# Performance work log

Hardware: AMD Instinct MI355X
Metric: run time of the kernel (lower is better)

## Reference

```python
import jax, jax.numpy as jnp
import numpy as np

IN_CH = 256
HID = 64
HEADS = 3 * 0 + 4  # num_heads


def setup_inputs() -> dict:
    key = jax.random.key(0)
    ks = jax.random.split(key, 5)
    B, C, H, W = 2, IN_CH, 64, 64
    x = jax.random.normal(ks[0], (B, C, H, W), dtype=jnp.float32)
    # per-head embed conv (kernel 1 -> stored as [heads, 3*HID, C]); kaiming fan_out-ish scale
    w_embed = jax.random.normal(ks[1], (HEADS, 3 * HID, C), dtype=jnp.float32) * np.float32(np.sqrt(2.0 / (3 * HID)))
    b_embed = jnp.zeros((HEADS, 3 * HID), dtype=jnp.float32)
    # output ConvTranspose2d(hidden*heads -> C, kernel 1): weight [hidden*heads, C]
    w_out = jax.random.normal(ks[2], (HEADS * HID, C), dtype=jnp.float32) * np.float32(np.sqrt(2.0 / C))
    b_out = jnp.zeros((C,), dtype=jnp.float32)
    return {"x": x, "w_embed": w_embed, "b_embed": b_embed, "w_out": w_out, "b_out": b_out}


def reference(x, w_embed, b_embed, w_out, b_out):
    B, C, H, W = x.shape
    N = H * W
    nH = w_embed.shape[0]
    D = w_embed.shape[1] // 3
    scale = D ** -0.5
    # 1x1 embed conv per head: [B, nH, 3D, N]
    xf = x.reshape(B, C, N)
    qkv = jnp.einsum('bcn,hdc->bhdn', xf, w_embed) + b_embed[None, :, :, None]
    q, k, v = jnp.split(qkv, 3, axis=2)  # each [B, nH, D, N]
    attn = jnp.einsum('bhci,bhcj->bhij', q, k) * scale  # [B, nH, N, N]
    attn = jax.nn.softmax(attn, axis=-1)
    y = jnp.einsum('bhij,bhcj->bhci', attn, v)  # [B, nH, D, N]
    y = y.reshape(B, nH * D, N)
    # output 1x1 transposed conv (kernel 1 == plain 1x1 projection)
    out = jnp.einsum('bkn,kc->bcn', y, w_out) + b_out[None, :, None]
    out = out.reshape(B, C, H, W)
    return out + x  # residual
```

## Files before the change

kernel.cpp:

```cpp
#include <hip/hip_runtime.h>
#include <hip/hip_bf16.h>

#define NH   4
#define D_   64
#define N_   4096
#define C_   256
#define ME   768
#define SPLITS 3

typedef float    f32x4  __attribute__((ext_vector_type(4)));
typedef float    f32x16 __attribute__((ext_vector_type(16)));
typedef _Float16 f16x8  __attribute__((ext_vector_type(8)));
typedef _Float16 f16x4  __attribute__((ext_vector_type(4)));
typedef _Float16 f16x2  __attribute__((ext_vector_type(2)));

__global__ __launch_bounds__(256) void xt_prep(const float* __restrict__ x,
                                               _Float16* __restrict__ xT) {
    __shared__ float T[64][68];
    const int n0 = blockIdx.x * 64, c0 = blockIdx.y * 64, b = blockIdx.z;
    const int t = threadIdx.x;
    const float* xp = x + ((size_t)b * C_ + c0) * N_ + n0;
    #pragma unroll
    for (int r = 0; r < 4; ++r) {
        int idx = r * 256 + t;
        int c = idx >> 4, ng = (idx & 15) * 4;
        *(f32x4*)&T[c][ng] = *(const f32x4*)(xp + (size_t)c * N_ + ng);
    }
    __syncthreads();
    _Float16* dp = xT + ((size_t)b * N_ + n0) * C_ + c0;
    #pragma unroll
    for (int r = 0; r < 2; ++r) {
        int idx = r * 256 + t;
        int n = idx >> 3, cg = (idx & 7) * 8;
        f16x8 v;
        #pragma unroll
        for (int j = 0; j < 8; ++j) v[j] = (_Float16)T[cg + j][n];
        *(f16x8*)(dp + (size_t)n * C_ + cg) = v;
    }
}

__global__ __launch_bounds__(256) void w_prep(const float* __restrict__ w_embed,
                                              const float* __restrict__ w_out,
                                              _Float16* __restrict__ wh,
                                              _Float16* __restrict__ w_outT) {
    __shared__ float T[64][68];
    const int t = threadIdx.x;
    if (blockIdx.x < 96) {
        int gid = blockIdx.x * 256 + t;
        const float* s = w_embed + (size_t)gid * 8;
        f32x4 a = *(const f32x4*)s, b2 = *(const f32x4*)(s + 4);
        f16x8 v = { (_Float16)a[0], (_Float16)a[1], (_Float16)a[2], (_Float16)a[3],
                    (_Float16)b2[0], (_Float16)b2[1], (_Float16)b2[2], (_Float16)b2[3] };
        *(f16x8*)(wh + (size_t)gid * 8) = v;
    } else {
        int tile = blockIdx.x - 96;
        int tc = tile & 3, tk = tile >> 2;
        #pragma unroll
        for (int r = 0; r < 4; ++r) {
            int idx = r * 256 + t;
            int kl = idx >> 4, cl = (idx & 15) * 4;
            *(f32x4*)&T[kl][cl] = *(const f32x4*)(w_out + (size_t)(tk * 64 + kl) * C_ + tc * 64 + cl);
        }
        __syncthreads();
        #pragma unroll
        for (int r = 0; r < 2; ++r) {
            int idx = r * 256 + t;
            int cl = idx >> 3, kg = (idx & 7) * 8;
            f16x8 v;
            #pragma unroll
            for (int j = 0; j < 8; ++j) v[j] = (_Float16)T[kg + j][cl];
            *(f16x8*)(w_outT + (size_t)(tc * 64 + cl) * C_ + tk * 64 + kg) = v;
        }
    }
}

__global__ __launch_bounds__(256) void qkv_gemm(const _Float16* __restrict__ xT,
                                                const _Float16* __restrict__ wh,
                                                const float* __restrict__ b_embed,
                                                _Float16* __restrict__ qT,
                                                _Float16* __restrict__ kT,
                                                _Float16* __restrict__ vB) {
    __shared__ __align__(16) union SM {
        struct { _Float16 A[64][40], X[64][40]; } s;
        float Os[64][68];
    } sm;
    const int n0 = blockIdx.x * 64, mt = blockIdx.y, b = blockIdx.z;
    const int m0 = mt * 64;
    const int t = threadIdx.x;
    const int lane = t & 63, w = t >> 6, quad = lane >> 4, l16 = lane & 15;
    const int srow = t >> 2, skoff = (t & 3) * 8;
    f32x4 acc[4] = {};
    for (int k0 = 0; k0 < C_; k0 += 32) {
        __syncthreads();
        *(f16x8*)&sm.s.A[srow][skoff] = *(const f16x8*)(wh + (size_t)(m0 + srow) * C_ + k0 + skoff);
        *(f16x8*)&sm.s.X[srow][skoff] = *(const f16x8*)(xT + ((size_t)b * N_ + n0 + srow) * C_ + k0 + skoff);
        __syncthreads();
        f16x8 af = *(const f16x8*)&sm.s.A[w * 16 + l16][quad * 8];
        #pragma unroll
        for (int nb = 0; nb < 4; ++nb) {
            f16x8 bf = *(const f16x8*)&sm.s.X[nb * 16 + l16][quad * 8];
            acc[nb] = __builtin_amdgcn_mfma_f32_16x16x32_f16(af, bf, acc[nb], 0, 0, 0);
        }
    }
    float bias[4];
    #pragma unroll
    for (int rg = 0; rg < 4; ++rg) bias[rg] = b_embed[m0 + w * 16 + quad * 4 + rg];
    __syncthreads();
    #pragma unroll
    for (int nb = 0; nb < 4; ++nb)
        #pragma unroll
        for (int rg = 0; rg < 4; ++rg)
            sm.Os[w * 16 + quad * 4 + rg][nb * 16 + l16] = acc[nb][rg] + bias[rg];
    __syncthreads();
    const int h = mt / 3, r3 = mt - h * 3;
    const int bh = b * NH + h;
    if (r3 < 2) {
        _Float16* dst = (r3 ? kT : qT) + ((size_t)bh * N_ + n0) * D_;
        #pragma unroll
        for (int r = 0; r < 2; ++r) {
            int idx = r * 256 + t;
            int n = idx >> 3, mg = (idx & 7) * 8;
            f16x8 v;
            #pragma unroll
            for (int j = 0; j < 8; ++j) v[j] = (_Float16)sm.Os[mg + j][n];
            *(f16x8*)(dst + (size_t)n * D_ + mg) = v;
        }
    } else {
        _Float16* dst = vB + (size_t)bh * D_ * N_ + n0;
        #pragma unroll
        for (int r = 0; r < 2; ++r) {
            int idx = r * 256 + t;
            int d = idx >> 3, ng = (idx & 7) * 8;
            f32x4 a = *(const f32x4*)&sm.Os[d][ng];
            f32x4 b2 = *(const f32x4*)&sm.Os[d][ng + 4];
            f16x8 v = { (_Float16)a[0], (_Float16)a[1], (_Float16)a[2], (_Float16)a[3],
                        (_Float16)b2[0], (_Float16)b2[1], (_Float16)b2[2], (_Float16)b2[3] };
            *(f16x8*)(dst + (size_t)d * N_ + ng) = v;
        }
    }
}

__global__ __launch_bounds__(256) void attn_kernel(const _Float16* __restrict__ qT,
                                                   const _Float16* __restrict__ kT,
                                                   const _Float16* __restrict__ vB,
                                                   _Float16* __restrict__ opart,
                                                   float* __restrict__ mpart,
                                                   float* __restrict__ lpart) {
    __shared__ __align__(16) union SM {
        struct { _Float16 K[64][76], V[64][76]; } s;
        _Float16 Os[128][76];
    } sm;
    const int t = threadIdx.x;
    const int qt = blockIdx.x, h = blockIdx.y;
    const int b = blockIdx.z / SPLITS, s = blockIdx.z % SPLITS;
    const int bh = b * NH + h, sbh = s * 8 + bh;
    const _Float16* kp = kT + (size_t)bh * N_ * D_;
    const _Float16* vp = vB + (size_t)bh * D_ * N_;
    const int lane = t & 63, w = t >> 6, l32 = lane & 31, hl = lane >> 5;
    const bool hl1 = (hl != 0);
    const int srow = t >> 3, scol = (t & 7) * 8;

    const _Float16* qp = qT + ((size_t)bh * N_ + qt * 128 + w * 32 + l32) * D_;
    f16x8 qf[4];
    #pragma unroll
    for (int kc = 0; kc < 4; ++kc) {
        qf[kc] = *(const f16x8*)(qp + kc * 16 + hl * 8);
        qf[kc] *= (_Float16)0.18033688f;
    }

    f32x16 oacc0 = {}, oacc1 = {};
    float m_run = -3.0e38f, l_run = 0.f;

    const int jt_lo = (s * 64) / SPLITS, jt_hi = ((s + 1) * 64) / SPLITS;
    f16x8 kpre[2], vpre[2];
    #pragma unroll
    for (int r = 0; r < 2; ++r) {
        int row = srow + r * 32;
        kpre[r] = *(const f16x8*)(kp + (size_t)(jt_lo * 64 + row) * D_ + scol);
        vpre[r] = *(const f16x8*)(vp + (size_t)row * N_ + jt_lo * 64 + scol);
    }

    for (int jt = jt_lo; jt < jt_hi; ++jt) {
        __syncthreads();
        #pragma unroll
        for (int r = 0; r < 2; ++r) {
            int row = srow + r * 32;
            *(f16x8*)&sm.s.K[row][scol] = kpre[r];
            *(f16x8*)&sm.s.V[row][scol] = vpre[r];
        }
        __syncthreads();
        if (jt + 1 < jt_hi) {
            #pragma unroll
            for (int r = 0; r < 2; ++r) {
                int row = srow + r * 32;
                kpre[r] = *(const f16x8*)(kp + (size_t)((jt + 1) * 64 + row) * D_ + scol);
                vpre[r] = *(const f16x8*)(vp + (size_t)row * N_ + (jt + 1) * 64 + scol);
            }
        }

        f32x16 sa0 = {}, sa1 = {};
        #pragma unroll
        for (int kc = 0; kc < 4; ++kc) {
            f16x8 kf0 = *(const f16x8*)&sm.s.K[l32][kc * 16 + hl * 8];
            sa0 = __builtin_amdgcn_mfma_f32_32x32x16_f16(kf0, qf[kc], sa0, 0, 0, 0);
            f16x8 kf1 = *(const f16x8*)&sm.s.K[32 + l32][kc * 16 + hl * 8];
            sa1 = __builtin_amdgcn_mfma_f32_32x32x16_f16(kf1, qf[kc], sa1, 0, 0, 0);
        }

        float mx = fmaxf(sa0[0], sa0[1]);
        #pragma unroll
        for (int r = 2; r < 16; ++r) mx = fmaxf(mx, sa0[r]);
        #pragma unroll
        for (int r = 0; r < 16; ++r) mx = fmaxf(mx, sa1[r]);
        mx = fmaxf(mx, __shfl_xor(mx, 32));
        float mnew  = fmaxf(m_run, mx);
        float alpha = exp2f(m_run - mnew);
        float rs = 0.f;
        #pragma unroll
        for (int r = 0; r < 16; ++r) { sa0[r] = exp2f(sa0[r] - mnew); rs += sa0[r]; }
        #pragma unroll
        for (int r = 0; r < 16; ++r) { sa1[r] = exp2f(sa1[r] - mnew); rs += sa1[r]; }
        rs += __shfl_xor(rs, 32);
        l_run = l_run * alpha + rs;
        m_run = mnew;
        #pragma unroll
        for (int r = 0; r < 16; ++r) { oacc0[r] *= alpha; oacc1[r] *= alpha; }

        #pragma unroll
        for (int jb = 0; jb < 2; ++jb) {
            const f32x16& sa = jb ? sa1 : sa0;
            int P[8], X[8];
            #pragma unroll
            for (int q = 0; q < 8; ++q) {
                f16x2 pk = { (_Float16)sa[2 * q], (_Float16)sa[2 * q + 1] };
                P[q] = __builtin_bit_cast(int, pk);
            }
            #pragma unroll
            for (int q = 0; q < 8; ++q) X[q] = __shfl_xor(P[q], 32);
            union FU { f16x8 v; int d[4]; } f0, f1;
            f0.d[0] = hl1 ? X[2] : P[0];
            f0.d[1] = hl1 ? X[3] : P[1];
            f0.d[2] = hl1 ? P[2] : X[0];
            f0.d[3] = hl1 ? P[3] : X[1];
            f1.d[0] = hl1 ? X[6] : P[4];
            f1.d[1] = hl1 ? X[7] : P[5];
            f1.d[2] = hl1 ? P[6] : X[4];
            f1.d[3] = hl1 ? P[7] : X[5];
            f16x8 vf = *(const f16x8*)&sm.s.V[l32][jb * 32 + hl * 8];
            oacc0 = __builtin_amdgcn_mfma_f32_32x32x16_f16(vf, f0.v, oacc0, 0, 0, 0);
            vf = *(const f16x8*)&sm.s.V[l32][jb * 32 + 16 + hl * 8];
            oacc0 = __builtin_amdgcn_mfma_f32_32x32x16_f16(vf, f1.v, oacc0, 0, 0, 0);
            vf = *(const f16x8*)&sm.s.V[32 + l32][jb * 32 + hl * 8];
            oacc1 = __builtin_amdgcn_mfma_f32_32x32x16_f16(vf, f0.v, oacc1, 0, 0, 0);
            vf = *(const f16x8*)&sm.s.V[32 + l32][jb * 32 + 16 + hl * 8];
            oacc1 = __builtin_amdgcn_mfma_f32_32x32x16_f16(vf, f1.v, oacc1, 0, 0, 0);
        }
    }

    float linv = 1.f / l_run;
    if (hl == 0) {
        mpart[(size_t)sbh * N_ + qt * 128 + w * 32 + l32] = m_run;
        lpart[(size_t)sbh * N_ + qt * 128 + w * 32 + l32] = l_run;
    }
    __syncthreads();
    #pragma unroll
    for (int db = 0; db < 2; ++db) {
        const f32x16& oc = db ? oacc1 : oacc0;
        #pragma unroll
        for (int rq = 0; rq < 4; ++rq) {
            f16x4 pv = { (_Float16)(oc[rq * 4 + 0] * linv), (_Float16)(oc[rq * 4 + 1] * linv),
                         (_Float16)(oc[rq * 4 + 2] * linv), (_Float16)(oc[rq * 4 + 3] * linv) };
            *(f16x4*)&sm.Os[w * 32 + l32][db * 32 + rq * 8 + hl * 4] = pv;
        }
    }
    __syncthreads();
    _Float16* op = opart + ((size_t)sbh * N_ + qt * 128) * D_;
    #pragma unroll
    for (int r = 0; r < 4; ++r) {
        int idx = r * 256 + t;
        int i = idx >> 3, ch = (idx & 7) * 8;
        *(f16x8*)(op + (size_t)i * D_ + ch) = *(const f16x8*)&sm.Os[i][ch];
    }
}

__global__ __launch_bounds__(256) void combine_kernel(const _Float16* __restrict__ opart,
                                                      const float* __restrict__ mpart,
                                                      const float* __restrict__ lpart,
                                                      _Float16* __restrict__ yT) {
    const int bhi = blockIdx.y;
    const int idx = blockIdx.x * 256 + threadIdx.x;
    const int n = idx >> 3, dg = (idx & 7) * 8;
    const int b = bhi >> 2, h = bhi & 3;
    float m0 = mpart[(size_t)bhi * N_ + n];
    float m1 = mpart[(size_t)(8 + bhi) * N_ + n];
    float m2 = mpart[(size_t)(16 + bhi) * N_ + n];
    float l0 = lpart[(size_t)bhi * N_ + n];
    float l1 = lpart[(size_t)(8 + bhi) * N_ + n];
    float l2 = lpart[(size_t)(16 + bhi) * N_ + n];
    float M  = fmaxf(m0, fmaxf(m1, m2));
    float w0 = exp2f(m0 - M) * l0, w1 = exp2f(m1 - M) * l1, w2 = exp2f(m2 - M) * l2;
    float inv = 1.f / (w0 + w1 + w2);
    w0 *= inv; w1 *= inv; w2 *= inv;
    f16x8 o0 = *(const f16x8*)(opart + ((size_t)bhi * N_ + n) * D_ + dg);
    f16x8 o1 = *(const f16x8*)(opart + ((size_t)(8 + bhi) * N_ + n) * D_ + dg);
    f16x8 o2 = *(const f16x8*)(opart + ((size_t)(16 + bhi) * N_ + n) * D_ + dg);
    f16x8 v;
    #pragma unroll
    for (int j = 0; j < 8; ++j)
        v[j] = (_Float16)(w0 * (float)o0[j] + w1 * (float)o1[j] + w2 * (float)o2[j]);
    *(f16x8*)(yT + ((size_t)b * N_ + n) * C_ + h * 64 + dg) = v;
}

__global__ __launch_bounds__(256) void proj_gemm(const _Float16* __restrict__ yT,
                                                 const _Float16* __restrict__ w_outT,
                                                 const float* __restrict__ b_out,
                                                 const float* __restrict__ x,
                                                 float* __restrict__ out) {
    __shared__ __align__(16) union SM {
        struct { _Float16 A[64][40], Y[64][40]; } s;
        float Os[64][68];
    } sm;
    const int n0 = blockIdx.x * 64, c0 = blockIdx.y * 64, b = blockIdx.z;
    const int t = threadIdx.x;
    const int lane = t & 63, w = t >> 6, quad = lane >> 4, l16 = lane & 15;
    const int srow = t >> 2, skoff = (t & 3) * 8;
    f32x4 acc[4] = {};
    for (int k0 = 0; k0 < C_; k0 += 32) {
        __syncthreads();
        *(f16x8*)&sm.s.A[srow][skoff] = *(const f16x8*)(w_outT + (size_t)(c0 + srow) * C_ + k0 + skoff);
        *(f16x8*)&sm.s.Y[srow][skoff] = *(const f16x8*)(yT + ((size_t)b * N_ + n0 + srow) * C_ + k0 + skoff);
        __syncthreads();
        f16x8 af = *(const f16x8*)&sm.s.A[w * 16 + l16][quad * 8];
        #pragma unroll
        for (int nb = 0; nb < 4; ++nb) {
            f16x8 bf = *(const f16x8*)&sm.s.Y[nb * 16 + l16][quad * 8];
            acc[nb] = __builtin_amdgcn_mfma_f32_16x16x32_f16(af, bf, acc[nb], 0, 0, 0);
        }
    }
    float bias[4];
    #pragma unroll
    for (int rg = 0; rg < 4; ++rg) bias[rg] = b_out[c0 + w * 16 + quad * 4 + rg];
    __syncthreads();
    #pragma unroll
    for (int nb = 0; nb < 4; ++nb)
        #pragma unroll
        for (int rg = 0; rg < 4; ++rg)
            sm.Os[w * 16 + quad * 4 + rg][nb * 16 + l16] = acc[nb][rg] + bias[rg];
    __syncthreads();
    const float* xp = x + ((size_t)b * C_ + c0) * N_ + n0;
    float* op = out + ((size_t)b * C_ + c0) * N_ + n0;
    #pragma unroll
    for (int r = 0; r < 4; ++r) {
        int idx = r * 256 + t;
        int c = idx >> 4, ng = (idx & 15) * 4;
        f32x4 v  = *(const f32x4*)&sm.Os[c][ng];
        f32x4 xv = *(const f32x4*)(xp + (size_t)c * N_ + ng);
        f32x4 o  = { v[0] + xv[0], v[1] + xv[1], v[2] + xv[2], v[3] + xv[3] };
        *(f32x4*)(op + (size_t)c * N_ + ng) = o;
    }
}

extern "C" void kernel_launch(void* const* d_in, const int* in_sizes, int n_in,
                              void* d_out, int out_size, void* d_ws, size_t ws_size,
                              hipStream_t stream) {
    const float* x       = (const float*)d_in[0];
    const float* w_embed = (const float*)d_in[1];
    const float* b_embed = (const float*)d_in[2];
    const float* w_out   = (const float*)d_in[3];
    const float* b_out   = (const float*)d_in[4];
    float* out = (float*)d_out;

    _Float16* base   = (_Float16*)d_ws;
    _Float16* xT     = base;
    _Float16* wh     = base + 2097152;
    _Float16* w_outT = base + 2293760;
    _Float16* qT     = base + 2359296;
    _Float16* kT     = base + 4456448;
    _Float16* vB     = base + 6553600;
    _Float16* yT     = base + 8650752;
    _Float16* opart  = base + 10747904;
    float*    mpart  = (float*)(base + 17039360);
    float*    lpart  = mpart + 98304;

    xt_prep       <<<dim3(64, 4, 2),  256, 0, stream>>>(x, xT);
    w_prep        <<<dim3(112, 1, 1), 256, 0, stream>>>(w_embed, w_out, wh, w_outT);
    qkv_gemm      <<<dim3(64, 12, 2), 256, 0, stream>>>(xT, wh, b_embed, qT, kT, vB);
    attn_kernel   <<<dim3(32, 4, 6),  256, 0, stream>>>(qT, kT, vB, opart, mpart, lpart);
    combine_kernel<<<dim3(128, 8, 1), 256, 0, stream>>>(opart, mpart, lpart, yT);
    proj_gemm     <<<dim3(64, 4, 2),  256, 0, stream>>>(yT, w_outT, b_out, x, out);
}
```

Baseline: 169.1 us.

## Fuse prep kernels, fold combine into projection, double-buffer attention K/V, split-4

```diff
diff --git a/kernel.cpp b/kernel.cpp
--- a/kernel.cpp
+++ b/kernel.cpp
@@ -6,54 +6,51 @@
 #define N_   4096
 #define C_   256
 #define ME   768
-#define SPLITS 3
+#define SPLITS 4
+#define QSCALE 0.18033688f
 
 typedef float    f32x4  __attribute__((ext_vector_type(4)));
 typedef float    f32x16 __attribute__((ext_vector_type(16)));
 typedef _Float16 f16x8  __attribute__((ext_vector_type(8)));
 typedef _Float16 f16x4  __attribute__((ext_vector_type(4)));
-typedef _Float16 f16x2  __attribute__((ext_vector_type(2)));
-
-__global__ __launch_bounds__(256) void xt_prep(const float* __restrict__ x,
-                                               _Float16* __restrict__ xT) {
+
+__global__ __launch_bounds__(256) void prep_kernel(const float* __restrict__ x,
+                                                   const float* __restrict__ w_embed,
+                                                   const float* __restrict__ w_out,
+                                                   _Float16* __restrict__ xT,
+                                                   _Float16* __restrict__ wh,
+                                                   _Float16* __restrict__ w_outT) {
     __shared__ float T[64][68];
-    const int n0 = blockIdx.x * 64, c0 = blockIdx.y * 64, b = blockIdx.z;
-    const int t = threadIdx.x;
-    const float* xp = x + ((size_t)b * C_ + c0) * N_ + n0;
-    #pragma unroll
-    for (int r = 0; r < 4; ++r) {
-        int idx = r * 256 + t;
-        int c = idx >> 4, ng = (idx & 15) * 4;
-        *(f32x4*)&T[c][ng] = *(const f32x4*)(xp + (size_t)c * N_ + ng);
-    }
-    __syncthreads();
-    _Float16* dp = xT + ((size_t)b * N_ + n0) * C_ + c0;
-    #pragma unroll
-    for (int r = 0; r < 2; ++r) {
-        int idx = r * 256 + t;
-        int n = idx >> 3, cg = (idx & 7) * 8;
-        f16x8 v;
-        #pragma unroll
-        for (int j = 0; j < 8; ++j) v[j] = (_Float16)T[cg + j][n];
-        *(f16x8*)(dp + (size_t)n * C_ + cg) = v;
-    }
-}
-
-__global__ __launch_bounds__(256) void w_prep(const float* __restrict__ w_embed,
-                                              const float* __restrict__ w_out,
-                                              _Float16* __restrict__ wh,
-                                              _Float16* __restrict__ w_outT) {
-    __shared__ float T[64][68];
-    const int t = threadIdx.x;
-    if (blockIdx.x < 96) {
-        int gid = blockIdx.x * 256 + t;
+    const int t = threadIdx.x, bx = blockIdx.x;
+    if (bx < 512) {
+        const int n0 = (bx & 63) * 64, c0 = ((bx >> 6) & 3) * 64, b = bx >> 8;
+        const float* xp = x + ((size_t)b * C_ + c0) * N_ + n0;
+        #pragma unroll
+        for (int r = 0; r < 4; ++r) {
+            int idx = r * 256 + t;
+            int c = idx >> 4, ng = (idx & 15) * 4;
+            *(f32x4*)&T[c][ng] = *(const f32x4*)(xp + (size_t)c * N_ + ng);
+        }
+        __syncthreads();
+        _Float16* dp = xT + ((size_t)b * N_ + n0) * C_ + c0;
+        #pragma unroll
+        for (int r = 0; r < 2; ++r) {
+            int idx = r * 256 + t;
+            int n = idx >> 3, cg = (idx & 7) * 8;
+            f16x8 v;
+            #pragma unroll
+            for (int j = 0; j < 8; ++j) v[j] = (_Float16)T[cg + j][n];
+            *(f16x8*)(dp + (size_t)n * C_ + cg) = v;
+        }
+    } else if (bx < 608) {
+        int gid = (bx - 512) * 256 + t;
         const float* s = w_embed + (size_t)gid * 8;
         f32x4 a = *(const f32x4*)s, b2 = *(const f32x4*)(s + 4);
         f16x8 v = { (_Float16)a[0], (_Float16)a[1], (_Float16)a[2], (_Float16)a[3],
                     (_Float16)b2[0], (_Float16)b2[1], (_Float16)b2[2], (_Float16)b2[3] };
         *(f16x8*)(wh + (size_t)gid * 8) = v;
     } else {
-        int tile = blockIdx.x - 96;
+        int tile = bx - 608;
         int tc = tile & 3, tk = tile >> 2;
         #pragma unroll
         for (int r = 0; r < 4; ++r) {
@@ -89,6 +86,8 @@
     const int t = threadIdx.x;
     const int lane = t & 63, w = t >> 6, quad = lane >> 4, l16 = lane & 15;
     const int srow = t >> 2, skoff = (t & 3) * 8;
+    const int h = mt / 3, r3 = mt - h * 3;
+    const float oscale = (r3 == 0) ? QSCALE : 1.0f;
     f32x4 acc[4] = {};
     for (int k0 = 0; k0 < C_; k0 += 32) {
         __syncthreads();
@@ -110,9 +109,8 @@
     for (int nb = 0; nb < 4; ++nb)
         #pragma unroll
         for (int rg = 0; rg < 4; ++rg)
-            sm.Os[w * 16 + quad * 4 + rg][nb * 16 + l16] = acc[nb][rg] + bias[rg];
-    __syncthreads();
-    const int h = mt / 3, r3 = mt - h * 3;
+            sm.Os[w * 16 + quad * 4 + rg][nb * 16 + l16] = (acc[nb][rg] + bias[rg]) * oscale;
+    __syncthreads();
     const int bh = b * NH + h;
     if (r3 < 2) {
         _Float16* dst = (r3 ? kT : qT) + ((size_t)bh * N_ + n0) * D_;
@@ -140,19 +138,19 @@
     }
 }
 
-__global__ __launch_bounds__(256) void attn_kernel(const _Float16* __restrict__ qT,
-                                                   const _Float16* __restrict__ kT,
-                                                   const _Float16* __restrict__ vB,
-                                                   _Float16* __restrict__ opart,
-                                                   float* __restrict__ mpart,
-                                                   float* __restrict__ lpart) {
+__global__ __launch_bounds__(256, 4) void attn_kernel(const _Float16* __restrict__ qT,
+                                                      const _Float16* __restrict__ kT,
+                                                      const _Float16* __restrict__ vB,
+                                                      _Float16* __restrict__ opart,
+                                                      float* __restrict__ mpart,
+                                                      float* __restrict__ lpart) {
     __shared__ __align__(16) union SM {
-        struct { _Float16 K[64][76], V[64][76]; } s;
+        struct { _Float16 K[2][64][76], V[2][64][76]; } s;
         _Float16 Os[128][76];
     } sm;
     const int t = threadIdx.x;
     const int qt = blockIdx.x, h = blockIdx.y;
-    const int b = blockIdx.z / SPLITS, s = blockIdx.z % SPLITS;
+    const int b = blockIdx.z >> 2, s = blockIdx.z & 3;
     const int bh = b * NH + h, sbh = s * 8 + bh;
     const _Float16* kp = kT + (size_t)bh * N_ * D_;
     const _Float16* vp = vB + (size_t)bh * D_ * N_;
@@ -163,15 +161,12 @@
     const _Float16* qp = qT + ((size_t)bh * N_ + qt * 128 + w * 32 + l32) * D_;
     f16x8 qf[4];
     #pragma unroll
-    for (int kc = 0; kc < 4; ++kc) {
-        qf[kc] = *(const f16x8*)(qp + kc * 16 + hl * 8);
-        qf[kc] *= (_Float16)0.18033688f;
-    }
+    for (int kc = 0; kc < 4; ++kc) qf[kc] = *(const f16x8*)(qp + kc * 16 + hl * 8);
 
     f32x16 oacc0 = {}, oacc1 = {};
     float m_run = -3.0e38f, l_run = 0.f;
 
-    const int jt_lo = (s * 64) / SPLITS, jt_hi = ((s + 1) * 64) / SPLITS;
+    const int jt_lo = s * 16, jt_hi = jt_lo + 16;
     f16x8 kpre[2], vpre[2];
     #pragma unroll
     for (int r = 0; r < 2; ++r) {
@@ -179,17 +174,18 @@
         kpre[r] = *(const f16x8*)(kp + (size_t)(jt_lo * 64 + row) * D_ + scol);
         vpre[r] = *(const f16x8*)(vp + (size_t)row * N_ + jt_lo * 64 + scol);
     }
-
+    #pragma unroll
+    for (int r = 0; r < 2; ++r) {
+        int row = srow + r * 32;
+        *(f16x8*)&sm.s.K[0][row][scol] = kpre[r];
+        *(f16x8*)&sm.s.V[0][row][scol] = vpre[r];
+    }
+
+    int buf = 0;
     for (int jt = jt_lo; jt < jt_hi; ++jt) {
         __syncthreads();
-        #pragma unroll
-        for (int r = 0; r < 2; ++r) {
-            int row = srow + r * 32;
-            *(f16x8*)&sm.s.K[row][scol] = kpre[r];
-            *(f16x8*)&sm.s.V[row][scol] = vpre[r];
-        }
-        __syncthreads();
-        if (jt + 1 < jt_hi) {
+        const bool more = (jt + 1 < jt_hi);
+        if (more) {
             #pragma unroll
             for (int r = 0; r < 2; ++r) {
                 int row = srow + r * 32;
@@ -201,40 +197,45 @@
         f32x16 sa0 = {}, sa1 = {};
         #pragma unroll
         for (int kc = 0; kc < 4; ++kc) {
-            f16x8 kf0 = *(const f16x8*)&sm.s.K[l32][kc * 16 + hl * 8];
+            f16x8 kf0 = *(const f16x8*)&sm.s.K[buf][l32][kc * 16 + hl * 8];
             sa0 = __builtin_amdgcn_mfma_f32_32x32x16_f16(kf0, qf[kc], sa0, 0, 0, 0);
-            f16x8 kf1 = *(const f16x8*)&sm.s.K[32 + l32][kc * 16 + hl * 8];
+            f16x8 kf1 = *(const f16x8*)&sm.s.K[buf][32 + l32][kc * 16 + hl * 8];
             sa1 = __builtin_amdgcn_mfma_f32_32x32x16_f16(kf1, qf[kc], sa1, 0, 0, 0);
         }
 
-        float mx = fmaxf(sa0[0], sa0[1]);
-        #pragma unroll
-        for (int r = 2; r < 16; ++r) mx = fmaxf(mx, sa0[r]);
-        #pragma unroll
-        for (int r = 0; r < 16; ++r) mx = fmaxf(mx, sa1[r]);
+        f32x16 mm;
+        #pragma unroll
+        for (int r = 0; r < 16; ++r) mm[r] = fmaxf(sa0[r], sa1[r]);
+        f32x4 m4;
+        #pragma unroll
+        for (int r = 0; r < 4; ++r)
+            m4[r] = fmaxf(fmaxf(mm[r], mm[r + 4]), fmaxf(mm[r + 8], mm[r + 12]));
+        float mx = fmaxf(fmaxf(m4[0], m4[1]), fmaxf(m4[2], m4[3]));
         mx = fmaxf(mx, __shfl_xor(mx, 32));
         float mnew  = fmaxf(m_run, mx);
         float alpha = exp2f(m_run - mnew);
-        float rs = 0.f;
-        #pragma unroll
-        for (int r = 0; r < 16; ++r) { sa0[r] = exp2f(sa0[r] - mnew); rs += sa0[r]; }
-        #pragma unroll
-        for (int r = 0; r < 16; ++r) { sa1[r] = exp2f(sa1[r] - mnew); rs += sa1[r]; }
+        #pragma unroll
+        for (int r = 0; r < 16; ++r) sa0[r] = exp2f(sa0[r] - mnew);
+        #pragma unroll
+        for (int r = 0; r < 16; ++r) sa1[r] = exp2f(sa1[r] - mnew);
+        f32x16 sv = sa0 + sa1;
+        f32x4 s4;
+        #pragma unroll
+        for (int r = 0; r < 4; ++r) s4[r] = (sv[r] + sv[r + 4]) + (sv[r + 8] + sv[r + 12]);
+        float rs = (s4[0] + s4[1]) + (s4[2] + s4[3]);
         rs += __shfl_xor(rs, 32);
         l_run = l_run * alpha + rs;
         m_run = mnew;
-        #pragma unroll
-        for (int r = 0; r < 16; ++r) { oacc0[r] *= alpha; oacc1[r] *= alpha; }
+        oacc0 *= alpha;
+        oacc1 *= alpha;
 
         #pragma unroll
         for (int jb = 0; jb < 2; ++jb) {
             const f32x16& sa = jb ? sa1 : sa0;
             int P[8], X[8];
             #pragma unroll
-            for (int q = 0; q < 8; ++q) {
-                f16x2 pk = { (_Float16)sa[2 * q], (_Float16)sa[2 * q + 1] };
-                P[q] = __builtin_bit_cast(int, pk);
-            }
+            for (int q = 0; q < 8; ++q)
+                P[q] = __builtin_bit_cast(int, __builtin_amdgcn_cvt_pkrtz(sa[2 * q], sa[2 * q + 1]));
             #pragma unroll
             for (int q = 0; q < 8; ++q) X[q] = __shfl_xor(P[q], 32);
             union FU { f16x8 v; int d[4]; } f0, f1;
@@ -246,15 +247,25 @@
             f1.d[1] = hl1 ? X[7] : P[5];
             f1.d[2] = hl1 ? P[6] : X[4];
             f1.d[3] = hl1 ? P[7] : X[5];
-            f16x8 vf = *(const f16x8*)&sm.s.V[l32][jb * 32 + hl * 8];
+            f16x8 vf = *(const f16x8*)&sm.s.V[buf][l32][jb * 32 + hl * 8];
             oacc0 = __builtin_amdgcn_mfma_f32_32x32x16_f16(vf, f0.v, oacc0, 0, 0, 0);
-            vf = *(const f16x8*)&sm.s.V[l32][jb * 32 + 16 + hl * 8];
+            vf = *(const f16x8*)&sm.s.V[buf][l32][jb * 32 + 16 + hl * 8];
             oacc0 = __builtin_amdgcn_mfma_f32_32x32x16_f16(vf, f1.v, oacc0, 0, 0, 0);
-            vf = *(const f16x8*)&sm.s.V[32 + l32][jb * 32 + hl * 8];
+            vf = *(const f16x8*)&sm.s.V[buf][32 + l32][jb * 32 + hl * 8];
             oacc1 = __builtin_amdgcn_mfma_f32_32x32x16_f16(vf, f0.v, oacc1, 0, 0, 0);
-            vf = *(const f16x8*)&sm.s.V[32 + l32][jb * 32 + 16 + hl * 8];
+            vf = *(const f16x8*)&sm.s.V[buf][32 + l32][jb * 32 + 16 + hl * 8];
             oacc1 = __builtin_amdgcn_mfma_f32_32x32x16_f16(vf, f1.v, oacc1, 0, 0, 0);
         }
+
+        if (more) {
+            #pragma unroll
+            for (int r = 0; r < 2; ++r) {
+                int row = srow + r * 32;
+                *(f16x8*)&sm.s.K[buf ^ 1][row][scol] = kpre[r];
+                *(f16x8*)&sm.s.V[buf ^ 1][row][scol] = vpre[r];
+            }
+        }
+        buf ^= 1;
     }
 
     float linv = 1.f / l_run;
@@ -283,52 +294,62 @@
     }
 }
 
-__global__ __launch_bounds__(256) void combine_kernel(const _Float16* __restrict__ opart,
-                                                      const float* __restrict__ mpart,
-                                                      const float* __restrict__ lpart,
-                                                      _Float16* __restrict__ yT) {
-    const int bhi = blockIdx.y;
-    const int idx = blockIdx.x * 256 + threadIdx.x;
-    const int n = idx >> 3, dg = (idx & 7) * 8;
-    const int b = bhi >> 2, h = bhi & 3;
-    float m0 = mpart[(size_t)bhi * N_ + n];
-    float m1 = mpart[(size_t)(8 + bhi) * N_ + n];
-    float m2 = mpart[(size_t)(16 + bhi) * N_ + n];
-    float l0 = lpart[(size_t)bhi * N_ + n];
-    float l1 = lpart[(size_t)(8 + bhi) * N_ + n];
-    float l2 = lpart[(size_t)(16 + bhi) * N_ + n];
-    float M  = fmaxf(m0, fmaxf(m1, m2));
-    float w0 = exp2f(m0 - M) * l0, w1 = exp2f(m1 - M) * l1, w2 = exp2f(m2 - M) * l2;
-    float inv = 1.f / (w0 + w1 + w2);
-    w0 *= inv; w1 *= inv; w2 *= inv;
-    f16x8 o0 = *(const f16x8*)(opart + ((size_t)bhi * N_ + n) * D_ + dg);
-    f16x8 o1 = *(const f16x8*)(opart + ((size_t)(8 + bhi) * N_ + n) * D_ + dg);
-    f16x8 o2 = *(const f16x8*)(opart + ((size_t)(16 + bhi) * N_ + n) * D_ + dg);
-    f16x8 v;
-    #pragma unroll
-    for (int j = 0; j < 8; ++j)
-        v[j] = (_Float16)(w0 * (float)o0[j] + w1 * (float)o1[j] + w2 * (float)o2[j]);
-    *(f16x8*)(yT + ((size_t)b * N_ + n) * C_ + h * 64 + dg) = v;
-}
-
-__global__ __launch_bounds__(256) void proj_gemm(const _Float16* __restrict__ yT,
+__global__ __launch_bounds__(256) void proj_gemm(const _Float16* __restrict__ opart,
+                                                 const float* __restrict__ mpart,
+                                                 const float* __restrict__ lpart,
                                                  const _Float16* __restrict__ w_outT,
                                                  const float* __restrict__ b_out,
                                                  const float* __restrict__ x,
                                                  float* __restrict__ out) {
     __shared__ __align__(16) union SM {
-        struct { _Float16 A[64][40], Y[64][40]; } s;
+        struct { _Float16 A[64][40], Y[64][40]; float W[4][64][4]; } s;
         float Os[64][68];
     } sm;
     const int n0 = blockIdx.x * 64, c0 = blockIdx.y * 64, b = blockIdx.z;
     const int t = threadIdx.x;
     const int lane = t & 63, w = t >> 6, quad = lane >> 4, l16 = lane & 15;
     const int srow = t >> 2, skoff = (t & 3) * 8;
+
+    {
+        const int nl = t & 63, hh = t >> 6;
+        const int bh = b * NH + hh;
+        float mv[4], lv[4];
+        #pragma unroll
+        for (int sI = 0; sI < 4; ++sI) {
+            mv[sI] = mpart[(size_t)(sI * 8 + bh) * N_ + n0 + nl];
+            lv[sI] = lpart[(size_t)(sI * 8 + bh) * N_ + n0 + nl];
+        }
+        float M = fmaxf(fmaxf(mv[0], mv[1]), fmaxf(mv[2], mv[3]));
+        float ws[4], sum = 0.f;
+        #pragma unroll
+        for (int sI = 0; sI < 4; ++sI) { ws[sI] = exp2f(mv[sI] - M) * lv[sI]; sum += ws[sI]; }
+        float inv = 1.f / sum;
+        #pragma unroll
+        for (int sI = 0; sI < 4; ++sI) sm.s.W[hh][nl][sI] = ws[sI] * inv;
+    }
+
     f32x4 acc[4] = {};
     for (int k0 = 0; k0 < C_; k0 += 32) {
         __syncthreads();
         *(f16x8*)&sm.s.A[srow][skoff] = *(const f16x8*)(w_outT + (size_t)(c0 + srow) * C_ + k0 + skoff);
-        *(f16x8*)&sm.s.Y[srow][skoff] = *(const f16x8*)(yT + ((size_t)b * N_ + n0 + srow) * C_ + k0 + skoff);
+        {
+            const int k = k0 + skoff;
+            const int hh = k >> 6, d0 = k & 63;
+            const int bh = b * NH + hh;
+            const float* Wn = &sm.s.W[hh][srow][0];
+            float accf[8] = {};
+            #pragma unroll
+            for (int sI = 0; sI < 4; ++sI) {
+                f16x8 ov = *(const f16x8*)(opart + ((size_t)(sI * 8 + bh) * N_ + n0 + srow) * D_ + d0);
+                float wsv = Wn[sI];
+                #pragma unroll
+                for (int j = 0; j < 8; ++j) accf[j] += wsv * (float)ov[j];
+            }
+            f16x8 yv;
+            #pragma unroll
+            for (int j = 0; j < 8; ++j) yv[j] = (_Float16)accf[j];
+            *(f16x8*)&sm.s.Y[srow][skoff] = yv;
+        }
         __syncthreads();
         f16x8 af = *(const f16x8*)&sm.s.A[w * 16 + l16][quad * 8];
         #pragma unroll
@@ -377,15 +398,12 @@
     _Float16* qT     = base + 2359296;
     _Float16* kT     = base + 4456448;
     _Float16* vB     = base + 6553600;
-    _Float16* yT     = base + 8650752;
-    _Float16* opart  = base + 10747904;
+    _Float16* opart  = base + 8650752;
     float*    mpart  = (float*)(base + 17039360);
-    float*    lpart  = mpart + 98304;
-
-    xt_prep       <<<dim3(64, 4, 2),  256, 0, stream>>>(x, xT);
-    w_prep        <<<dim3(112, 1, 1), 256, 0, stream>>>(w_embed, w_out, wh, w_outT);
-    qkv_gemm      <<<dim3(64, 12, 2), 256, 0, stream>>>(xT, wh, b_embed, qT, kT, vB);
-    attn_kernel   <<<dim3(32, 4, 6),  256, 0, stream>>>(qT, kT, vB, opart, mpart, lpart);
-    combine_kernel<<<dim3(128, 8, 1), 256, 0, stream>>>(opart, mpart, lpart, yT);
-    proj_gemm     <<<dim3(64, 4, 2),  256, 0, stream>>>(yT, w_outT, b_out, x, out);
+    float*    lpart  = mpart + 131072;
+
+    prep_kernel<<<dim3(624, 1, 1), 256, 0, stream>>>(x, w_embed, w_out, xT, wh, w_outT);
+    qkv_gemm   <<<dim3(64, 12, 2), 256, 0, stream>>>(xT, wh, b_embed, qT, kT, vB);
+    attn_kernel<<<dim3(32, 4, 8),  256, 0, stream>>>(qT, kT, vB, opart, mpart, lpart);
+    proj_gemm  <<<dim3(64, 4, 2),  256, 0, stream>>>(opart, mpart, lpart, w_outT, b_out, x, out);
 }
```

Measured after the change: 166.3 us. Within noise of the previous version (-1.7%).
